# Optimization experiments

Measured on AMD Instinct MI355X. Metric: run time of the kernel, lower is better.

## Reference

```python
import jax, jax.numpy as jnp
import numpy as np

B, N, D, H = 2, 64, 256, 8
DK = D // H
EPS = 1e-5


def layer_norm(x, g, b):
    mu = jnp.mean(x, axis=-1, keepdims=True)
    var = jnp.var(x, axis=-1, keepdims=True)
    return (x - mu) * jax.lax.rsqrt(var + EPS) * g + b


def setup_inputs() -> dict:
    key = jax.random.key(0)
    ks = jax.random.split(key, 12)
    s = 1.0 / np.sqrt(D)
    inp = {
        "x": jax.random.normal(ks[0], (B, N, N, D), jnp.float32),
        "W_lk": jax.random.uniform(ks[1], (D, D), jnp.float32, -s, s),
        "W_rk": jax.random.uniform(ks[2], (D, D), jnp.float32, -s, s),
        "W_lv": jax.random.uniform(ks[3], (D, D), jnp.float32, -s, s),
        "W_rv": jax.random.uniform(ks[4], (D, D), jnp.float32, -s, s),
        "W_out": jax.random.uniform(ks[5], (D, D), jnp.float32, -s, s),
        "ln_agg_g": jnp.ones((D,), jnp.float32),
        "ln_agg_b": jnp.zeros((D,), jnp.float32),
        "W1": jax.random.uniform(ks[6], (D, 2 * D), jnp.float32, -s, s),
        "b1": jnp.zeros((2 * D,), jnp.float32),
        "W2": jax.random.uniform(ks[7], (2 * D, D), jnp.float32, -1.0 / np.sqrt(2 * D), 1.0 / np.sqrt(2 * D)),
        "b2": jnp.zeros((D,), jnp.float32),
        "ln2_g": jnp.ones((D,), jnp.float32),
        "ln2_b": jnp.zeros((D,), jnp.float32),
    }
    return inp


def reference(x, W_lk, W_rk, W_lv, W_rv, W_out, ln_agg_g, ln_agg_b, W1, b1, W2, b2, ln2_g, ln2_b):
    b, n = x.shape[0], x.shape[1]
    # projections (no bias), split into heads: [b, n, n, H, DK]
    lk = (x @ W_lk).reshape(b, n, n, H, DK)
    rk = (x @ W_rk).reshape(b, n, n, H, DK)
    lv = (x @ W_lv).reshape(b, n, n, H, DK)
    rv = (x @ W_rv).reshape(b, n, n, H, DK)
    # triangle attention scores over intermediate node 'a'
    scores = jnp.einsum('bxahd,bayhd->bxayh', lk, rk) / np.sqrt(DK)
    att = jax.nn.softmax(scores, axis=2)
    # fused triangle value aggregation: sum_a att * lv[x,a] * rv[a,y]
    o = jnp.einsum('bxayh,bxahd,bayhd->bxyhd', att, lv, rv)
    o = o.reshape(b, n, n, D) @ W_out
    # FFN block (dropout = 0)
    h = layer_norm(x + o, ln_agg_g, ln_agg_b)
    m = jax.nn.relu(h @ W1 + b1) @ W2 + b2
    return layer_norm(m + h, ln2_g, ln2_b)
```

## Files before the change

kernel.cpp:

```cpp
#include <hip/hip_runtime.h>

#define ROWS 8192
#define DIM  256

typedef short short8 __attribute__((ext_vector_type(8)));
typedef float f4     __attribute__((ext_vector_type(4)));

__device__ __forceinline__ float bf2f(unsigned int u16) {
    union { unsigned int i; float f; } v;
    v.i = (u16 & 0xffffu) << 16;
    return v.f;
}
__device__ __forceinline__ unsigned short f2bf(float f) {
    union { float f; unsigned int u; } v; v.f = f;
    unsigned int r = v.u + 0x7fffu + ((v.u >> 16) & 1u);
    return (unsigned short)(r >> 16);
}

__global__ __launch_bounds__(256)
void cast_all(const float* __restrict__ x, unsigned short* __restrict__ xb,
              const float* __restrict__ w0, const float* __restrict__ w1,
              const float* __restrict__ w2, const float* __restrict__ w3,
              const float* __restrict__ w4, const float* __restrict__ w5,
              const float* __restrict__ w6, unsigned short* __restrict__ wt)
{
    if (blockIdx.x < 2048) {
        const size_t i = ((size_t)blockIdx.x * 256 + threadIdx.x) * 4;
        float4 v = *(const float4*)(x + i);
        uint2 p;
        p.x = f2bf(v.x) | ((unsigned int)f2bf(v.y) << 16);
        p.y = f2bf(v.z) | ((unsigned int)f2bf(v.w) << 16);
        *(uint2*)(xb + i) = p;
        return;
    }
    __shared__ float t[32][33];
    int id = blockIdx.x - 2048;
    const float* src; int K, N, Ntiles; size_t doff;
    if (id < 320) {
        int w = id >> 6; id &= 63; K = 256; N = 256; Ntiles = 8;
        doff = (size_t)w * 65536;
        src = (w == 0) ? w0 : (w == 1) ? w1 : (w == 2) ? w2 : (w == 3) ? w3 : w4;
    } else if (id < 448) {
        id -= 320; K = 256; N = 512; Ntiles = 16; doff = 327680; src = w5;
    } else {
        id -= 448; K = 512; N = 256; Ntiles = 8;  doff = 458752; src = w6;
    }
    const int tk = id / Ntiles, tn = id % Ntiles;
    const int k0 = tk * 32, n0 = tn * 32;
    const int c = threadIdx.x & 31, r8 = threadIdx.x >> 5;
    for (int rr = r8; rr < 32; rr += 8)
        t[rr][c] = src[(size_t)(k0 + rr) * N + n0 + c];
    __syncthreads();
    for (int rr = r8; rr < 32; rr += 8)
        wt[doff + (size_t)(n0 + rr) * K + k0 + c] = f2bf(t[c][rr]);
}

__global__ __launch_bounds__(256)
void proj_mfma(const unsigned short* __restrict__ A, const unsigned short* __restrict__ WT,
               unsigned short* __restrict__ projT)
{
    const int lane = threadIdx.x & 63, wave = threadIdx.x >> 6;
    const int wsel = blockIdx.x >> 2;
    const int col0 = (blockIdx.x & 3) * 64;
    const int m0 = blockIdx.y * 128 + wave * 32;
    const int lm = lane & 15, lk8 = (lane >> 4) * 8;
    const unsigned short* W = WT + (size_t)wsel * 65536;
    unsigned short* dst = projT + (size_t)wsel * 2097152;

    f4 acc[2][4];
    #pragma unroll
    for (int i = 0; i < 2; ++i)
        #pragma unroll
        for (int j = 0; j < 4; ++j) acc[i][j] = (f4){0.f, 0.f, 0.f, 0.f};

    #pragma unroll 2
    for (int kc = 0; kc < 256; kc += 32) {
        short8 af[2], bf[4];
        #pragma unroll
        for (int i = 0; i < 2; ++i)
            af[i] = *(const short8*)(A + (size_t)(m0 + i * 16 + lm) * 256 + kc + lk8);
        #pragma unroll
        for (int j = 0; j < 4; ++j)
            bf[j] = *(const short8*)(W + (size_t)(col0 + j * 16 + lm) * 256 + kc + lk8);
        #pragma unroll
        for (int i = 0; i < 2; ++i)
            #pragma unroll
            for (int j = 0; j < 4; ++j)
                acc[i][j] = __builtin_amdgcn_mfma_f32_16x16x32_bf16(af[i], bf[j], acc[i][j], 0, 0, 0);
    }

    const int rbase = (lane >> 4) * 4;
    const int swap = (wsel == 3);
    #pragma unroll
    for (int i = 0; i < 2; ++i)
        #pragma unroll
        for (int j = 0; j < 4; ++j) {
            const int c = col0 + j * 16 + lm;
            const int h = c >> 5, d = c & 31;
            #pragma unroll
            for (int r = 0; r < 4; ++r) {
                const int m = m0 + i * 16 + rbase + r;
                const int b = m >> 12, ii = (m >> 6) & 63, jj = m & 63;
                const int p = swap ? jj : ii;
                const int q = swap ? ii : jj;
                const size_t idx = ((((size_t)b * 8 + h) * 64 + p) * 64 + q) * 32 + d;
                dst[idx] = f2bf(acc[i][j][r]);
            }
        }
}

__global__ __launch_bounds__(256)
void scores_mfma(const unsigned short* __restrict__ lkT, const unsigned short* __restrict__ rkT,
                 unsigned short* __restrict__ S)
{
    const int lane = threadIdx.x & 63, wave = threadIdx.x >> 6;
    const int bi = blockIdx.x;
    const int b = bi >> 7, h = (bi >> 4) & 7, a = (bi & 15) * 4 + wave;
    const size_t bh = (size_t)b * 8 + h;
    const int lm = lane & 15, lk8 = (lane >> 4) * 8;

    short8 af[4], bf[4];
    #pragma unroll
    for (int t = 0; t < 4; ++t) {
        af[t] = *(const short8*)(lkT + ((bh * 64 + (t * 16 + lm)) * 64 + a) * 32 + lk8);
        bf[t] = *(const short8*)(rkT + ((bh * 64 + a) * 64 + (t * 16 + lm)) * 32 + lk8);
    }
    const int rbase = (lane >> 4) * 4;
    unsigned short* Sb = S + bh * 262144 + a * 64;
    #pragma unroll
    for (int mt = 0; mt < 4; ++mt)
        #pragma unroll
        for (int nt = 0; nt < 4; ++nt) {
            f4 acc = (f4){0.f, 0.f, 0.f, 0.f};
            acc = __builtin_amdgcn_mfma_f32_16x16x32_bf16(af[mt], bf[nt], acc, 0, 0, 0);
            #pragma unroll
            for (int r = 0; r < 4; ++r) {
                const int xx = mt * 16 + rbase + r;
                const int yy = nt * 16 + lm;
                Sb[(size_t)xx * 4096 + yy] = f2bf(acc[r] * 0.17677669529663687f);
            }
        }
}

__global__ __launch_bounds__(256)
void softmax_agg(const unsigned short* __restrict__ S, const unsigned short* __restrict__ lvT,
                 const unsigned short* __restrict__ rvT, unsigned short* __restrict__ obuf)
{
    __shared__ float att[64][64];
    __shared__ float lvL[64][32];
    __shared__ float smx[4][64], ssm[4][64], invL[64];
    const int bi = blockIdx.x;
    const int b = bi >> 9, h = (bi >> 6) & 7, x = bi & 63;
    const size_t bh = (size_t)b * 8 + h;
    const int tid = threadIdx.x;

    {
        const int a = tid >> 2, yo = (tid & 3) * 16;
        const unsigned short* Sp = S + (bh * 64 + x) * 4096 + a * 64 + yo;
        uint4 p0 = *(const uint4*)(Sp);
        uint4 p1 = *(const uint4*)(Sp + 8);
        att[a][yo +  0] = bf2f(p0.x); att[a][yo +  1] = bf2f(p0.x >> 16);
        att[a][yo +  2] = bf2f(p0.y); att[a][yo +  3] = bf2f(p0.y >> 16);
        att[a][yo +  4] = bf2f(p0.z); att[a][yo +  5] = bf2f(p0.z >> 16);
        att[a][yo +  6] = bf2f(p0.w); att[a][yo +  7] = bf2f(p0.w >> 16);
        att[a][yo +  8] = bf2f(p1.x); att[a][yo +  9] = bf2f(p1.x >> 16);
        att[a][yo + 10] = bf2f(p1.y); att[a][yo + 11] = bf2f(p1.y >> 16);
        att[a][yo + 12] = bf2f(p1.z); att[a][yo + 13] = bf2f(p1.z >> 16);
        att[a][yo + 14] = bf2f(p1.w); att[a][yo + 15] = bf2f(p1.w >> 16);
        const int d0 = (tid & 3) * 8;
        uint4 q = *(const uint4*)(lvT + ((bh * 64 + x) * 64 + a) * 32 + d0);
        lvL[a][d0 + 0] = bf2f(q.x); lvL[a][d0 + 1] = bf2f(q.x >> 16);
        lvL[a][d0 + 2] = bf2f(q.y); lvL[a][d0 + 3] = bf2f(q.y >> 16);
        lvL[a][d0 + 4] = bf2f(q.z); lvL[a][d0 + 5] = bf2f(q.z >> 16);
        lvL[a][d0 + 6] = bf2f(q.w); lvL[a][d0 + 7] = bf2f(q.w >> 16);
    }
    __syncthreads();

    {
        const int y = tid & 63, az = tid >> 6;
        float mx = -1e30f;
        for (int a = az; a < 64; a += 4) mx = fmaxf(mx, att[a][y]);
        smx[az][y] = mx;
    }
    __syncthreads();

    {
        const int y = tid & 63, az = tid >> 6;
        const float mx = fmaxf(fmaxf(smx[0][y], smx[1][y]), fmaxf(smx[2][y], smx[3][y]));
        float s = 0.f;
        for (int a = az; a < 64; a += 4) {
            float e = __expf(att[a][y] - mx);
            att[a][y] = e;
            s += e;
        }
        ssm[az][y] = s;
    }
    __syncthreads();
    if (tid < 64)
        invL[tid] = 1.f / (ssm[0][tid] + ssm[1][tid] + ssm[2][tid] + ssm[3][tid]);
    __syncthreads();

    {
        const int dp = tid & 15, yb = tid >> 4;
        #pragma unroll
        for (int it = 0; it < 4; ++it) {
            const int y = yb + it * 16;
            const unsigned short* rvr = rvT + (bh * 64 + y) * 2048 + dp * 2;
            float a0 = 0.f, a1 = 0.f;
            #pragma unroll 8
            for (int a = 0; a < 64; ++a) {
                unsigned int pk = *(const unsigned int*)(rvr + a * 32);
                float w = att[a][y];
                a0 = fmaf(w * lvL[a][2 * dp],     bf2f(pk),       a0);
                a1 = fmaf(w * lvL[a][2 * dp + 1], bf2f(pk >> 16), a1);
            }
            const float inv = invL[y];
            a0 *= inv; a1 *= inv;
            unsigned int st = f2bf(a0) | ((unsigned int)f2bf(a1) << 16);
            *(unsigned int*)(obuf + (((size_t)b * 64 + x) * 64 + y) * 256 + h * 32 + dp * 2) = st;
        }
    }
}

__global__ __launch_bounds__(256)
void gemm_ffn1(const unsigned short* __restrict__ A, const unsigned short* __restrict__ WT,
               const float* __restrict__ bias, unsigned short* __restrict__ outB)
{
    constexpr int K = 256, N = 512;
    const int lane = threadIdx.x & 63, wave = threadIdx.x >> 6;
    const int m0 = blockIdx.y * 128 + wave * 32;
    const int col0 = blockIdx.x * 64;
    const int lm = lane & 15, lk8 = (lane >> 4) * 8;

    f4 acc[2][4];
    #pragma unroll
    for (int i = 0; i < 2; ++i)
        #pragma unroll
        for (int j = 0; j < 4; ++j) acc[i][j] = (f4){0.f, 0.f, 0.f, 0.f};

    #pragma unroll 2
    for (int kc = 0; kc < K; kc += 32) {
        short8 af[2], bf[4];
        #pragma unroll
        for (int i = 0; i < 2; ++i)
            af[i] = *(const short8*)(A + (size_t)(m0 + i * 16 + lm) * K + kc + lk8);
        #pragma unroll
        for (int j = 0; j < 4; ++j)
            bf[j] = *(const short8*)(WT + (size_t)(col0 + j * 16 + lm) * K + kc + lk8);
        #pragma unroll
        for (int i = 0; i < 2; ++i)
            #pragma unroll
            for (int j = 0; j < 4; ++j)
                acc[i][j] = __builtin_amdgcn_mfma_f32_16x16x32_bf16(af[i], bf[j], acc[i][j], 0, 0, 0);
    }

    const int rbase = (lane >> 4) * 4;
    #pragma unroll
    for (int i = 0; i < 2; ++i)
        #pragma unroll
        for (int j = 0; j < 4; ++j) {
            const int n = col0 + j * 16 + lm;
            const float bb = bias[n];
            #pragma unroll
            for (int r = 0; r < 4; ++r) {
                const int m = m0 + i * 16 + rbase + r;
                outB[(size_t)m * N + n] = f2bf(fmaxf(acc[i][j][r] + bb, 0.f));
            }
        }
}

template<int K, bool RBF16, bool OBF16>
__global__ __launch_bounds__(256)
void gemm_ln_t(const unsigned short* __restrict__ A, const unsigned short* __restrict__ WT,
               const float* __restrict__ bias, const void* __restrict__ resid,
               const float* __restrict__ gamma, const float* __restrict__ beta,
               void* __restrict__ out)
{
    __shared__ float ps[16][4], pq[16][4];
    const int lane = threadIdx.x & 63, wave = threadIdx.x >> 6;
    const int m0 = blockIdx.x * 16;
    const int col0 = wave * 64;
    const int lm = lane & 15, lk8 = (lane >> 4) * 8;

    f4 acc[4];
    #pragma unroll
    for (int j = 0; j < 4; ++j) acc[j] = (f4){0.f, 0.f, 0.f, 0.f};

    #pragma unroll 2
    for (int kc = 0; kc < K; kc += 32) {
        short8 af = *(const short8*)(A + (size_t)(m0 + lm) * K + kc + lk8);
        #pragma unroll
        for (int j = 0; j < 4; ++j) {
            short8 bf = *(const short8*)(WT + (size_t)(col0 + j * 16 + lm) * K + kc + lk8);
            acc[j] = __builtin_amdgcn_mfma_f32_16x16x32_bf16(af, bf, acc[j], 0, 0, 0);
        }
    }

    const int rbase = (lane >> 4) * 4;
    float v[4][4];
    float s[4] = {0.f, 0.f, 0.f, 0.f}, q[4] = {0.f, 0.f, 0.f, 0.f};
    #pragma unroll
    for (int j = 0; j < 4; ++j) {
        const int n = col0 + j * 16 + lm;
        const float bb = bias ? bias[n] : 0.f;
        #pragma unroll
        for (int r = 0; r < 4; ++r) {
            const int m = m0 + rbase + r;
            const size_t idx = (size_t)m * 256 + n;
            const float rr = RBF16 ? bf2f(((const unsigned short*)resid)[idx])
                                   : ((const float*)resid)[idx];
            float t = acc[j][r] + bb + rr;
            v[j][r] = t;
            s[r] += t;
            q[r] = fmaf(t, t, q[r]);
        }
    }
    #pragma unroll
    for (int off = 1; off < 16; off <<= 1) {
        #pragma unroll
        for (int r = 0; r < 4; ++r) {
            s[r] += __shfl_xor(s[r], off);
            q[r] += __shfl_xor(q[r], off);
        }
    }
    if (lm == 0) {
        #pragma unroll
        for (int r = 0; r < 4; ++r) {
            ps[rbase + r][wave] = s[r];
            pq[rbase + r][wave] = q[r];
        }
    }
    __syncthreads();
    #pragma unroll
    for (int r = 0; r < 4; ++r) {
        const int lr = rbase + r;
        const float Sm = ps[lr][0] + ps[lr][1] + ps[lr][2] + ps[lr][3];
        const float Qm = pq[lr][0] + pq[lr][1] + pq[lr][2] + pq[lr][3];
        const float mu = Sm * (1.f / 256.f);
        const float ri = rsqrtf(Qm * (1.f / 256.f) - mu * mu + 1e-5f);
        const int m = m0 + lr;
        #pragma unroll
        for (int j = 0; j < 4; ++j) {
            const int n = col0 + j * 16 + lm;
            const size_t idx = (size_t)m * 256 + n;
            const float rv = (v[j][r] - mu) * ri * gamma[n] + beta[n];
            if (OBF16) ((unsigned short*)out)[idx] = f2bf(rv);
            else       ((float*)out)[idx] = rv;
        }
    }
}

extern "C" void kernel_launch(void* const* d_in, const int* in_sizes, int n_in,
                              void* d_out, int out_size, void* d_ws, size_t ws_size,
                              hipStream_t stream)
{
    const float* x    = (const float*)d_in[0];
    const float* Wlk  = (const float*)d_in[1];
    const float* Wrk  = (const float*)d_in[2];
    const float* Wlv  = (const float*)d_in[3];
    const float* Wrv  = (const float*)d_in[4];
    const float* Wout = (const float*)d_in[5];
    const float* g1   = (const float*)d_in[6];
    const float* be1  = (const float*)d_in[7];
    const float* W1   = (const float*)d_in[8];
    const float* b1   = (const float*)d_in[9];
    const float* W2   = (const float*)d_in[10];
    const float* b2   = (const float*)d_in[11];
    const float* g2   = (const float*)d_in[12];
    const float* be2  = (const float*)d_in[13];

    char* base = (char*)d_ws;
    const size_t MB = 1ull << 20;
    unsigned short* xb    = (unsigned short*)(base + 0);
    unsigned short* obufb = (unsigned short*)(base + 0);
    unsigned short* projT = (unsigned short*)(base + 4 * MB);
    unsigned short* lkT   = projT;
    unsigned short* rkT   = projT + 2097152;
    unsigned short* lvT   = projT + 2 * 2097152;
    unsigned short* rvT   = projT + 3 * 2097152;
    unsigned short* hb    = (unsigned short*)(base + 20 * MB);
    unsigned short* midb  = (unsigned short*)(base + 24 * MB);
    unsigned short* Sbuf  = (unsigned short*)(base + 32 * MB);
    unsigned short* WT    = (unsigned short*)(base + 40 * MB);

    cast_all<<<2624, 256, 0, stream>>>(x, xb, Wlk, Wrk, Wlv, Wrv, Wout, W1, W2, WT);
    proj_mfma<<<dim3(16, 64), 256, 0, stream>>>(xb, WT, projT);
    scores_mfma<<<256, 256, 0, stream>>>(lkT, rkT, Sbuf);
    softmax_agg<<<1024, 256, 0, stream>>>(Sbuf, lvT, rvT, obufb);
    gemm_ln_t<256, false, true><<<512, 256, 0, stream>>>(obufb, WT + 262144, nullptr, x, g1, be1, hb);
    gemm_ffn1<<<dim3(8, 64), 256, 0, stream>>>(hb, WT + 327680, b1, midb);
    gemm_ln_t<512, true, false><<<512, 256, 0, stream>>>(midb, WT + 458752, b2, hb, g2, be2, (float*)d_out);
}
```

Measured before the change: 188.2 us.

## Fuse output projection, LayerNorm, and FFN into one kernel using LDS

Replaces three kernels (W_out GEMM with LN, FFN1 GEMM with ReLU, FFN2 GEMM with LN) with one kernel. Each 16-row block keeps the intermediate h and the 512-wide hidden activations in swizzled shared memory, so the hb and midb global round-trips and two launches go away. The cost is less parallelism in the FFN1 stage (512 blocks of 16 rows instead of 512 tiles of 128x64), and each block re-reads full W1/W2 from L2.

```diff
diff --git a/kernel.cpp b/kernel.cpp
--- a/kernel.cpp
+++ b/kernel.cpp
@@ -222,130 +222,166 @@
     }
 }
 
+__device__ __forceinline__ int swz8(int r, int c, int rl) {
+    return r * rl + ((((c >> 3) ^ (r & 7)) << 3) | (c & 7));
+}
+
 __global__ __launch_bounds__(256)
-void gemm_ffn1(const unsigned short* __restrict__ A, const unsigned short* __restrict__ WT,
-               const float* __restrict__ bias, unsigned short* __restrict__ outB)
-{
-    constexpr int K = 256, N = 512;
-    const int lane = threadIdx.x & 63, wave = threadIdx.x >> 6;
-    const int m0 = blockIdx.y * 128 + wave * 32;
-    const int col0 = blockIdx.x * 64;
-    const int lm = lane & 15, lk8 = (lane >> 4) * 8;
-
-    f4 acc[2][4];
-    #pragma unroll
-    for (int i = 0; i < 2; ++i)
-        #pragma unroll
-        for (int j = 0; j < 4; ++j) acc[i][j] = (f4){0.f, 0.f, 0.f, 0.f};
-
-    #pragma unroll 2
-    for (int kc = 0; kc < K; kc += 32) {
-        short8 af[2], bf[4];
-        #pragma unroll
-        for (int i = 0; i < 2; ++i)
-            af[i] = *(const short8*)(A + (size_t)(m0 + i * 16 + lm) * K + kc + lk8);
-        #pragma unroll
-        for (int j = 0; j < 4; ++j)
-            bf[j] = *(const short8*)(WT + (size_t)(col0 + j * 16 + lm) * K + kc + lk8);
-        #pragma unroll
-        for (int i = 0; i < 2; ++i)
-            #pragma unroll
-            for (int j = 0; j < 4; ++j)
-                acc[i][j] = __builtin_amdgcn_mfma_f32_16x16x32_bf16(af[i], bf[j], acc[i][j], 0, 0, 0);
-    }
-
-    const int rbase = (lane >> 4) * 4;
-    #pragma unroll
-    for (int i = 0; i < 2; ++i)
-        #pragma unroll
-        for (int j = 0; j < 4; ++j) {
-            const int n = col0 + j * 16 + lm;
-            const float bb = bias[n];
-            #pragma unroll
-            for (int r = 0; r < 4; ++r) {
-                const int m = m0 + i * 16 + rbase + r;
-                outB[(size_t)m * N + n] = f2bf(fmaxf(acc[i][j][r] + bb, 0.f));
-            }
-        }
-}
-
-template<int K, bool RBF16, bool OBF16>
-__global__ __launch_bounds__(256)
-void gemm_ln_t(const unsigned short* __restrict__ A, const unsigned short* __restrict__ WT,
-               const float* __restrict__ bias, const void* __restrict__ resid,
-               const float* __restrict__ gamma, const float* __restrict__ beta,
-               void* __restrict__ out)
-{
+void ffn_fused(const unsigned short* __restrict__ A,
+               const unsigned short* __restrict__ WoT,
+               const unsigned short* __restrict__ W1T,
+               const unsigned short* __restrict__ W2T,
+               const float* __restrict__ xres,
+               const float* __restrict__ g1, const float* __restrict__ be1,
+               const float* __restrict__ b1, const float* __restrict__ b2,
+               const float* __restrict__ g2, const float* __restrict__ be2,
+               float* __restrict__ out)
+{
+    __shared__ unsigned short hs[16 * 256];
+    __shared__ unsigned short ms[16 * 512];
     __shared__ float ps[16][4], pq[16][4];
     const int lane = threadIdx.x & 63, wave = threadIdx.x >> 6;
     const int m0 = blockIdx.x * 16;
+    const int lm = lane & 15, lk8 = (lane >> 4) * 8;
+    const int rbase = (lane >> 4) * 4;
     const int col0 = wave * 64;
-    const int lm = lane & 15, lk8 = (lane >> 4) * 8;
-
-    f4 acc[4];
-    #pragma unroll
-    for (int j = 0; j < 4; ++j) acc[j] = (f4){0.f, 0.f, 0.f, 0.f};
-
-    #pragma unroll 2
-    for (int kc = 0; kc < K; kc += 32) {
-        short8 af = *(const short8*)(A + (size_t)(m0 + lm) * K + kc + lk8);
-        #pragma unroll
-        for (int j = 0; j < 4; ++j) {
-            short8 bf = *(const short8*)(WT + (size_t)(col0 + j * 16 + lm) * K + kc + lk8);
-            acc[j] = __builtin_amdgcn_mfma_f32_16x16x32_bf16(af, bf, acc[j], 0, 0, 0);
-        }
-    }
-
-    const int rbase = (lane >> 4) * 4;
-    float v[4][4];
-    float s[4] = {0.f, 0.f, 0.f, 0.f}, q[4] = {0.f, 0.f, 0.f, 0.f};
-    #pragma unroll
-    for (int j = 0; j < 4; ++j) {
-        const int n = col0 + j * 16 + lm;
-        const float bb = bias ? bias[n] : 0.f;
-        #pragma unroll
-        for (int r = 0; r < 4; ++r) {
-            const int m = m0 + rbase + r;
-            const size_t idx = (size_t)m * 256 + n;
-            const float rr = RBF16 ? bf2f(((const unsigned short*)resid)[idx])
-                                   : ((const float*)resid)[idx];
-            float t = acc[j][r] + bb + rr;
-            v[j][r] = t;
-            s[r] += t;
-            q[r] = fmaf(t, t, q[r]);
-        }
-    }
-    #pragma unroll
-    for (int off = 1; off < 16; off <<= 1) {
-        #pragma unroll
-        for (int r = 0; r < 4; ++r) {
-            s[r] += __shfl_xor(s[r], off);
-            q[r] += __shfl_xor(q[r], off);
-        }
-    }
-    if (lm == 0) {
-        #pragma unroll
-        for (int r = 0; r < 4; ++r) {
-            ps[rbase + r][wave] = s[r];
-            pq[rbase + r][wave] = q[r];
-        }
-    }
-    __syncthreads();
-    #pragma unroll
-    for (int r = 0; r < 4; ++r) {
-        const int lr = rbase + r;
-        const float Sm = ps[lr][0] + ps[lr][1] + ps[lr][2] + ps[lr][3];
-        const float Qm = pq[lr][0] + pq[lr][1] + pq[lr][2] + pq[lr][3];
-        const float mu = Sm * (1.f / 256.f);
-        const float ri = rsqrtf(Qm * (1.f / 256.f) - mu * mu + 1e-5f);
-        const int m = m0 + lr;
+    float hreg[4][4];
+
+    {
+        f4 acc[4];
+        #pragma unroll
+        for (int j = 0; j < 4; ++j) acc[j] = (f4){0.f, 0.f, 0.f, 0.f};
+        #pragma unroll 2
+        for (int kc = 0; kc < 256; kc += 32) {
+            short8 af = *(const short8*)(A + (size_t)(m0 + lm) * 256 + kc + lk8);
+            #pragma unroll
+            for (int j = 0; j < 4; ++j) {
+                short8 bf = *(const short8*)(WoT + (size_t)(col0 + j * 16 + lm) * 256 + kc + lk8);
+                acc[j] = __builtin_amdgcn_mfma_f32_16x16x32_bf16(af, bf, acc[j], 0, 0, 0);
+            }
+        }
+        float v[4][4], s[4] = {0.f, 0.f, 0.f, 0.f}, q[4] = {0.f, 0.f, 0.f, 0.f};
         #pragma unroll
         for (int j = 0; j < 4; ++j) {
             const int n = col0 + j * 16 + lm;
-            const size_t idx = (size_t)m * 256 + n;
-            const float rv = (v[j][r] - mu) * ri * gamma[n] + beta[n];
-            if (OBF16) ((unsigned short*)out)[idx] = f2bf(rv);
-            else       ((float*)out)[idx] = rv;
+            #pragma unroll
+            for (int r = 0; r < 4; ++r) {
+                const float t = acc[j][r] + xres[(size_t)(m0 + rbase + r) * 256 + n];
+                v[j][r] = t;
+                s[r] += t;
+                q[r] = fmaf(t, t, q[r]);
+            }
+        }
+        #pragma unroll
+        for (int off = 1; off < 16; off <<= 1)
+            #pragma unroll
+            for (int r = 0; r < 4; ++r) {
+                s[r] += __shfl_xor(s[r], off);
+                q[r] += __shfl_xor(q[r], off);
+            }
+        if (lm == 0)
+            #pragma unroll
+            for (int r = 0; r < 4; ++r) {
+                ps[rbase + r][wave] = s[r];
+                pq[rbase + r][wave] = q[r];
+            }
+        __syncthreads();
+        #pragma unroll
+        for (int r = 0; r < 4; ++r) {
+            const int lr = rbase + r;
+            const float Sm = ps[lr][0] + ps[lr][1] + ps[lr][2] + ps[lr][3];
+            const float Qm = pq[lr][0] + pq[lr][1] + pq[lr][2] + pq[lr][3];
+            const float mu = Sm * (1.f / 256.f);
+            const float ri = rsqrtf(Qm * (1.f / 256.f) - mu * mu + 1e-5f);
+            #pragma unroll
+            for (int j = 0; j < 4; ++j) {
+                const int n = col0 + j * 16 + lm;
+                const unsigned short hb16 = f2bf((v[j][r] - mu) * ri * g1[n] + be1[n]);
+                hs[swz8(lr, n, 256)] = hb16;
+                hreg[j][r] = bf2f(hb16);
+            }
+        }
+    }
+    __syncthreads();
+
+    {
+        const int c0 = wave * 128;
+        f4 acc2[8];
+        #pragma unroll
+        for (int j = 0; j < 8; ++j) acc2[j] = (f4){0.f, 0.f, 0.f, 0.f};
+        #pragma unroll 2
+        for (int kc = 0; kc < 256; kc += 32) {
+            short8 af = *(const short8*)(hs + swz8(lm, kc + lk8, 256));
+            #pragma unroll
+            for (int j = 0; j < 8; ++j) {
+                short8 bf = *(const short8*)(W1T + (size_t)(c0 + j * 16 + lm) * 256 + kc + lk8);
+                acc2[j] = __builtin_amdgcn_mfma_f32_16x16x32_bf16(af, bf, acc2[j], 0, 0, 0);
+            }
+        }
+        #pragma unroll
+        for (int j = 0; j < 8; ++j) {
+            const int n = c0 + j * 16 + lm;
+            const float bb = b1[n];
+            #pragma unroll
+            for (int r = 0; r < 4; ++r)
+                ms[swz8(rbase + r, n, 512)] = f2bf(fmaxf(acc2[j][r] + bb, 0.f));
+        }
+    }
+    __syncthreads();
+
+    {
+        f4 acc[4];
+        #pragma unroll
+        for (int j = 0; j < 4; ++j) acc[j] = (f4){0.f, 0.f, 0.f, 0.f};
+        #pragma unroll 2
+        for (int kc = 0; kc < 512; kc += 32) {
+            short8 af = *(const short8*)(ms + swz8(lm, kc + lk8, 512));
+            #pragma unroll
+            for (int j = 0; j < 4; ++j) {
+                short8 bf = *(const short8*)(W2T + (size_t)(col0 + j * 16 + lm) * 512 + kc + lk8);
+                acc[j] = __builtin_amdgcn_mfma_f32_16x16x32_bf16(af, bf, acc[j], 0, 0, 0);
+            }
+        }
+        float v[4][4], s[4] = {0.f, 0.f, 0.f, 0.f}, q[4] = {0.f, 0.f, 0.f, 0.f};
+        #pragma unroll
+        for (int j = 0; j < 4; ++j) {
+            const int n = col0 + j * 16 + lm;
+            const float bb = b2[n];
+            #pragma unroll
+            for (int r = 0; r < 4; ++r) {
+                const float t = acc[j][r] + bb + hreg[j][r];
+                v[j][r] = t;
+                s[r] += t;
+                q[r] = fmaf(t, t, q[r]);
+            }
+        }
+        #pragma unroll
+        for (int off = 1; off < 16; off <<= 1)
+            #pragma unroll
+            for (int r = 0; r < 4; ++r) {
+                s[r] += __shfl_xor(s[r], off);
+                q[r] += __shfl_xor(q[r], off);
+            }
+        if (lm == 0)
+            #pragma unroll
+            for (int r = 0; r < 4; ++r) {
+                ps[rbase + r][wave] = s[r];
+                pq[rbase + r][wave] = q[r];
+            }
+        __syncthreads();
+        #pragma unroll
+        for (int r = 0; r < 4; ++r) {
+            const int lr = rbase + r;
+            const float Sm = ps[lr][0] + ps[lr][1] + ps[lr][2] + ps[lr][3];
+            const float Qm = pq[lr][0] + pq[lr][1] + pq[lr][2] + pq[lr][3];
+            const float mu = Sm * (1.f / 256.f);
+            const float ri = rsqrtf(Qm * (1.f / 256.f) - mu * mu + 1e-5f);
+            const int m = m0 + lr;
+            #pragma unroll
+            for (int j = 0; j < 4; ++j) {
+                const int n = col0 + j * 16 + lm;
+                out[(size_t)m * 256 + n] = (v[j][r] - mu) * ri * g2[n] + be2[n];
+            }
         }
     }
 }
@@ -378,8 +414,6 @@
     unsigned short* rkT   = projT + 2097152;
     unsigned short* lvT   = projT + 2 * 2097152;
     unsigned short* rvT   = projT + 3 * 2097152;
-    unsigned short* hb    = (unsigned short*)(base + 20 * MB);
-    unsigned short* midb  = (unsigned short*)(base + 24 * MB);
     unsigned short* Sbuf  = (unsigned short*)(base + 32 * MB);
     unsigned short* WT    = (unsigned short*)(base + 40 * MB);
 
@@ -387,7 +421,6 @@
     proj_mfma<<<dim3(16, 64), 256, 0, stream>>>(xb, WT, projT);
     scores_mfma<<<256, 256, 0, stream>>>(lkT, rkT, Sbuf);
     softmax_agg<<<1024, 256, 0, stream>>>(Sbuf, lvT, rvT, obufb);
-    gemm_ln_t<256, false, true><<<512, 256, 0, stream>>>(obufb, WT + 262144, nullptr, x, g1, be1, hb);
-    gemm_ffn1<<<dim3(8, 64), 256, 0, stream>>>(hb, WT + 327680, b1, midb);
-    gemm_ln_t<512, true, false><<<512, 256, 0, stream>>>(midb, WT + 458752, b2, hb, g2, be2, (float*)d_out);
-}
+    ffn_fused<<<512, 256, 0, stream>>>(obufb, WT + 262144, WT + 327680, WT + 458752,
+                                       x, g1, be1, b1, b2, g2, be2, (float*)d_out);
+}
```

After: 183.4 us. 1.03x faster.
